# Performance work log

Measured on AMD Instinct MI355X. Metric: run time of the kernel, lower is better.

Reference implementation:

```python
import math
import jax
import jax.numpy as jnp
import numpy as np
from jax import lax
from jax.scipy.special import digamma

EPS_RHO = 1e-12
EPS_LOG = 1e-8
BANDWIDTH_FACTOR = 1.06
MIN_BANDWIDTH = 1e-4


def setup_inputs() -> dict:
    key = jax.random.key(0)
    activity = jax.random.uniform(key, (1024, 64), dtype=jnp.float32)  # values in [0,1]
    return {"activity": activity, "k": 5}


def _knn_joint_entropy(activity, k):
    B, N = activity.shape
    # (B, B, N) pairwise differences -> squared distances (B, B)
    diff = activity[:, None, :] - activity[None, :, :]
    dists_sq = jnp.sum(diff * diff, axis=-1)
    # k+1 smallest per row (includes self-distance 0); torch.topk(largest=False) ascending
    neg_topk, _ = lax.top_k(-dists_sq, k + 1)
    rho_sq = jnp.maximum(-neg_topk[:, k], EPS_RHO)
    # log unit-ball volume via lgamma (avoids overflow for large N)
    log_c_d = 0.5 * N * math.log(math.pi) - math.lgamma(N / 2 + 1)
    dg_k = digamma(jnp.float32(k))
    dg_B = digamma(jnp.float32(B))
    log_rho_sum = 0.5 * jnp.mean(jnp.log(rho_sq))
    h_nats = -dg_k + dg_B + log_c_d + N * log_rho_sum
    return h_nats / math.log(2.0)


def _kde_density(samples, query_points, bandwidth_factor):
    B_samples, R = samples.shape
    std = jnp.std(samples, axis=0, ddof=1)  # torch.std uses unbiased (ddof=1)
    h = jnp.maximum(bandwidth_factor * std * B_samples ** (-0.2), MIN_BANDWIDTH)  # (R,)
    X = query_points[:, None, :]  # (B, 1, R)
    Y = samples[None, :, :]       # (1, B, R)
    hr = h[None, None, :]
    norm_factor = math.sqrt(2 * math.pi)
    u_orig = (X - Y) / hr
    u_left = (X + Y) / hr
    u_right = (X - (2.0 - Y)) / hr
    kernel = (jnp.exp(-0.5 * u_orig ** 2)
              + jnp.exp(-0.5 * u_left ** 2)
              + jnp.exp(-0.5 * u_right ** 2)) / norm_factor
    density = jnp.sum(kernel, axis=1) / (B_samples * h[None, :])  # (B, R)
    return density


def _kde_marginal_entropies(activity, bandwidth_factor):
    density = _kde_density(activity, activity, bandwidth_factor)
    log_prob = jnp.log(density + EPS_LOG)
    return -jnp.mean(log_prob, axis=0)  # (R,)


def reference(activity, k):
    joint_h = _knn_joint_entropy(activity, k)            # scalar (bits)
    marginals = _kde_marginal_entropies(activity, BANDWIDTH_FACTOR)  # (N,)
    return jnp.concatenate([joint_h[None], marginals])   # (N+1,)
```

## Files before the change

### kernel.cpp

```cpp
#include <hip/hip_runtime.h>
#include <math.h>

#define BB 1024
#define NN 64

#define LN2F 0.69314718055994530942f
#define BINS 256
#define TW   64
#define HSIZE 769
#define NOUT 258
#define OBASE 255

__global__ __launch_bounds__(256, 4) void fused_kernel(const float* __restrict__ act,
                                                       const int* __restrict__ kptr,
                                                       float* __restrict__ logrho,
                                                       float* __restrict__ partial) {
    const int bx = blockIdx.x;
    const int tid = threadIdx.x;

    __shared__ float s_d[4096];
    __shared__ float s_x[264];

    if (bx < 256) {
        const int qbase = bx * 4;
        if (tid < 64) {
            ((float4*)s_x)[tid] = ((const float4*)(act + (size_t)qbase * NN))[tid];
        }
        __syncthreads();

        #pragma unroll 1
        for (int c = 0; c < 4; ++c) {
            const int j = tid + 256 * c;
            const float4* row = (const float4*)(act + (size_t)j * NN);
            float a0 = 0.f, a1 = 0.f, a2 = 0.f, a3 = 0.f;
            #pragma unroll 2
            for (int d = 0; d < 16; ++d) {
                const float4 v = row[d];
                {   const float4 qq = ((const float4*)s_x)[d];
                    float x0 = v.x - qq.x, x1 = v.y - qq.y, x2 = v.z - qq.z, x3 = v.w - qq.w;
                    a0 += x0 * x0 + x1 * x1 + x2 * x2 + x3 * x3; }
                {   const float4 qq = ((const float4*)s_x)[16 + d];
                    float x0 = v.x - qq.x, x1 = v.y - qq.y, x2 = v.z - qq.z, x3 = v.w - qq.w;
                    a1 += x0 * x0 + x1 * x1 + x2 * x2 + x3 * x3; }
                {   const float4 qq = ((const float4*)s_x)[32 + d];
                    float x0 = v.x - qq.x, x1 = v.y - qq.y, x2 = v.z - qq.z, x3 = v.w - qq.w;
                    a2 += x0 * x0 + x1 * x1 + x2 * x2 + x3 * x3; }
                {   const float4 qq = ((const float4*)s_x)[48 + d];
                    float x0 = v.x - qq.x, x1 = v.y - qq.y, x2 = v.z - qq.z, x3 = v.w - qq.w;
                    a3 += x0 * x0 + x1 * x1 + x2 * x2 + x3 * x3; }
            }
            s_d[0 * 1024 + j] = a0;
            s_d[1 * 1024 + j] = a1;
            s_d[2 * 1024 + j] = a2;
            s_d[3 * 1024 + j] = a3;
        }
        __syncthreads();

        const int w = tid >> 6, lane = tid & 63;
        float v[16];
        #pragma unroll
        for (int c = 0; c < 16; ++c) v[c] = s_d[w * 1024 + lane + 64 * c];
        const int kk = kptr[0];
        float last = 0.f;
        for (int e = 0; e <= kk; ++e) {
            float bv = 1e30f; int bi = 0;
            #pragma unroll
            for (int c = 0; c < 16; ++c) { if (v[c] < bv) { bv = v[c]; bi = c; } }
            float mv = bv; int mi = (lane << 4) | bi;
            #pragma unroll
            for (int off = 32; off > 0; off >>= 1) {
                float ov = __shfl_xor(mv, off);
                int   oi = __shfl_xor(mi, off);
                if (ov < mv || (ov == mv && oi < mi)) { mv = ov; mi = oi; }
            }
            last = mv;
            if ((mi >> 4) == lane) v[mi & 15] = 1e30f;
        }
        if (lane == 0) {
            logrho[qbase + w] = __builtin_amdgcn_logf(fmaxf(last, 1e-12f)) * LN2F;
        }
    } else {
        const int idx = bx - 256;
        const int r = idx >> 2;
        const int chunk = idx & 3;

        int*   hint = (int*)s_d;
        float* harr = s_d;
        float* ktab = s_d + 772;
        float* outg = s_d + 840;

        float cv[4];
        float lsum = 0.f, lsq = 0.f;
        #pragma unroll
        for (int c = 0; c < 4; ++c) {
            const int j = tid + 256 * c;
            float v = act[(size_t)j * NN + r];
            cv[c] = v;
            lsum += v; lsq += v * v;
        }
        #pragma unroll
        for (int off = 32; off > 0; off >>= 1) {
            lsum += __shfl_xor(lsum, off);
            lsq  += __shfl_xor(lsq,  off);
        }
        const int wid = tid >> 6;
        if ((tid & 63) == 0) { s_x[wid] = lsum; s_x[4 + wid] = lsq; }

        for (int i = tid; i < HSIZE; i += 256) hint[i] = 0;
        __syncthreads();

        const float total = s_x[0] + s_x[1] + s_x[2] + s_x[3];
        const float totsq = s_x[4] + s_x[5] + s_x[6] + s_x[7];
        const float mean = total * (1.f / BB);
        const float var = (totsq - (float)BB * mean * mean) * (1.f / (BB - 1));
        const float stdv = sqrtf(fmaxf(var, 0.f));
        const float h = fmaxf(1.06f * 0.25f * stdv, 1e-4f);
        const float ih = 1.f / h;
        const float a  = 0.84932180028801904272f * ih;
        const float ad = a * (1.f / (float)BINS);

        #pragma unroll
        for (int c = 0; c < 4; ++c) {
            const float x = cv[c];
            int b0 = (int)floorf(x * (float)BINS) + BINS;
            int b1 = (int)floorf(-x * (float)BINS) + BINS;
            int b2 = (int)floorf((2.f - x) * (float)BINS) + BINS;
            b0 = min(max(b0, 0), HSIZE - 1);
            b1 = min(max(b1, 0), HSIZE - 1);
            b2 = min(max(b2, 0), HSIZE - 1);
            atomicAdd(&hint[b0], 1);
            atomicAdd(&hint[b1], 1);
            atomicAdd(&hint[b2], 1);
        }
        if (tid <= TW) {
            const float t = ad * (float)tid;
            ktab[tid] = __builtin_amdgcn_exp2f(-(t * t));
        }
        __syncthreads();

        for (int i = tid; i < HSIZE; i += 256) {
            const int c = hint[i];
            harr[i] = (float)c;
        }
        __syncthreads();

        for (int o = tid; o < NOUT; o += 256) {
            const float* hp = harr + OBASE + o;
            float acc = hp[0] * ktab[0];
            #pragma unroll 4
            for (int m = 1; m <= TW; ++m)
                acc += (hp[m] + hp[-m]) * ktab[m];
            outg[o] = acc;
        }
        __syncthreads();

        const float dscale = 0.39894228040143267794f * ih * (1.f / (float)BB);
        const float x = cv[chunk];
        const float u = fmaf(x, (float)BINS, (float)OBASE + 0.5f);
        const float fu = floorf(u);
        const int i0 = (int)fu - OBASE;
        const float f = u - fu;
        const float dv = outg[i0] + (outg[i0 + 1] - outg[i0]) * f;
        float lp = __builtin_amdgcn_logf(fmaf(dv, dscale, 1e-8f)) * LN2F;

        #pragma unroll
        for (int off = 32; off > 0; off >>= 1) lp += __shfl_xor(lp, off);
        if ((tid & 63) == 0) s_x[8 + wid] = lp;
        __syncthreads();
        if (tid == 0) {
            partial[idx] = s_x[8] + s_x[9] + s_x[10] + s_x[11];
        }
    }
}

__global__ __launch_bounds__(256) void finalize_kernel(const float* __restrict__ logrho,
                                                       const float* __restrict__ partial,
                                                       const int* __restrict__ kptr,
                                                       double log_c_d, double dg_B,
                                                       float* __restrict__ out) {
    const int tid = threadIdx.x;
    __shared__ double red[256];

    double s = 0.0;
    #pragma unroll
    for (int c = 0; c < 4; ++c) s += (double)logrho[tid + 256 * c];
    red[tid] = s;
    __syncthreads();
    for (int st = 128; st > 0; st >>= 1) { if (tid < st) red[tid] += red[tid + st]; __syncthreads(); }

    if (tid == 0) {
        const int kk = kptr[0];
        double dgk = -0.57721566490153286061;
        for (int t = 1; t < kk; ++t) dgk += 1.0 / (double)t;
        const double log_rho_sum = 0.5 * (red[0] / (double)BB);
        const double h_nats = -dgk + dg_B + log_c_d + (double)NN * log_rho_sum;
        out[0] = (float)(h_nats / 0.69314718055994530942);
    }
    if (tid < NN) {
        const float p = partial[tid * 4 + 0] + partial[tid * 4 + 1]
                      + partial[tid * 4 + 2] + partial[tid * 4 + 3];
        out[1 + tid] = -p * (1.0f / (float)BB);
    }
}

extern "C" void kernel_launch(void* const* d_in, const int* in_sizes, int n_in,
                              void* d_out, int out_size, void* d_ws, size_t ws_size,
                              hipStream_t stream) {
    const float* act = (const float*)d_in[0];
    const int* kptr = (const int*)d_in[1];
    float* out = (float*)d_out;

    float* logrho = (float*)d_ws;
    float* partial = logrho + BB;

    const double log_c_d = 0.5 * (double)NN * log(M_PI) - lgamma((double)NN / 2.0 + 1.0);
    const double xB = (double)BB;
    const double dg_B = log(xB) - 1.0 / (2.0 * xB) - 1.0 / (12.0 * xB * xB)
                        + 1.0 / (120.0 * xB * xB * xB * xB);

    fused_kernel<<<512, 256, 0, stream>>>(act, kptr, logrho, partial);
    finalize_kernel<<<1, 256, 0, stream>>>(logrho, partial, kptr, log_c_d, dg_B, out);
}
```

Baseline: 22.58 us.

## Fold finalize into main kernel via last-block atomic counter; interleave row loads

Removes the separate finalize kernel launch. Each block increments a global counter, and the last block to finish does the final reduction, reading the per-block values through atomic loads. A memsetAsync is added to reset the counter. The distance loop is also restructured so each thread loads four rows in the same iteration with float4 accumulators, instead of four sequential passes, to expose more memory-level parallelism at the cost of more registers.

```diff
diff --git a/kernel.cpp b/kernel.cpp
--- a/kernel.cpp
+++ b/kernel.cpp
@@ -11,10 +11,15 @@
 #define NOUT 258
 #define OBASE 255
 
+#define NBLOCKS 512
+
 __global__ __launch_bounds__(256, 4) void fused_kernel(const float* __restrict__ act,
                                                        const int* __restrict__ kptr,
                                                        float* __restrict__ logrho,
-                                                       float* __restrict__ partial) {
+                                                       float* __restrict__ partial,
+                                                       int* __restrict__ counter,
+                                                       float* __restrict__ out,
+                                                       double log_c_d, double dg_B) {
     const int bx = blockIdx.x;
     const int tid = threadIdx.x;
 
@@ -28,32 +33,52 @@
         }
         __syncthreads();
 
-        #pragma unroll 1
-        for (int c = 0; c < 4; ++c) {
-            const int j = tid + 256 * c;
-            const float4* row = (const float4*)(act + (size_t)j * NN);
-            float a0 = 0.f, a1 = 0.f, a2 = 0.f, a3 = 0.f;
-            #pragma unroll 2
-            for (int d = 0; d < 16; ++d) {
-                const float4 v = row[d];
-                {   const float4 qq = ((const float4*)s_x)[d];
-                    float x0 = v.x - qq.x, x1 = v.y - qq.y, x2 = v.z - qq.z, x3 = v.w - qq.w;
-                    a0 += x0 * x0 + x1 * x1 + x2 * x2 + x3 * x3; }
-                {   const float4 qq = ((const float4*)s_x)[16 + d];
-                    float x0 = v.x - qq.x, x1 = v.y - qq.y, x2 = v.z - qq.z, x3 = v.w - qq.w;
-                    a1 += x0 * x0 + x1 * x1 + x2 * x2 + x3 * x3; }
-                {   const float4 qq = ((const float4*)s_x)[32 + d];
-                    float x0 = v.x - qq.x, x1 = v.y - qq.y, x2 = v.z - qq.z, x3 = v.w - qq.w;
-                    a2 += x0 * x0 + x1 * x1 + x2 * x2 + x3 * x3; }
-                {   const float4 qq = ((const float4*)s_x)[48 + d];
-                    float x0 = v.x - qq.x, x1 = v.y - qq.y, x2 = v.z - qq.z, x3 = v.w - qq.w;
-                    a3 += x0 * x0 + x1 * x1 + x2 * x2 + x3 * x3; }
-            }
-            s_d[0 * 1024 + j] = a0;
-            s_d[1 * 1024 + j] = a1;
-            s_d[2 * 1024 + j] = a2;
-            s_d[3 * 1024 + j] = a3;
-        }
+        const float4* qf = (const float4*)s_x;
+        float4 acc0 = {0,0,0,0}, acc1 = {0,0,0,0}, acc2 = {0,0,0,0}, acc3 = {0,0,0,0};
+        const float4* row0 = (const float4*)(act + (size_t)(tid + 0)   * NN);
+        const float4* row1 = (const float4*)(act + (size_t)(tid + 256) * NN);
+        const float4* row2 = (const float4*)(act + (size_t)(tid + 512) * NN);
+        const float4* row3 = (const float4*)(act + (size_t)(tid + 768) * NN);
+
+        #pragma unroll 2
+        for (int d = 0; d < 16; ++d) {
+            const float4 q0 = qf[d];
+            const float4 q1 = qf[16 + d];
+            const float4 q2 = qf[32 + d];
+            const float4 q3 = qf[48 + d];
+            {   const float4 v = row0[d];
+                float x,y,z,w;
+                x=v.x-q0.x; y=v.y-q0.y; z=v.z-q0.z; w=v.w-q0.w; acc0.x += x*x+y*y+z*z+w*w;
+                x=v.x-q1.x; y=v.y-q1.y; z=v.z-q1.z; w=v.w-q1.w; acc0.y += x*x+y*y+z*z+w*w;
+                x=v.x-q2.x; y=v.y-q2.y; z=v.z-q2.z; w=v.w-q2.w; acc0.z += x*x+y*y+z*z+w*w;
+                x=v.x-q3.x; y=v.y-q3.y; z=v.z-q3.z; w=v.w-q3.w; acc0.w += x*x+y*y+z*z+w*w; }
+            {   const float4 v = row1[d];
+                float x,y,z,w;
+                x=v.x-q0.x; y=v.y-q0.y; z=v.z-q0.z; w=v.w-q0.w; acc1.x += x*x+y*y+z*z+w*w;
+                x=v.x-q1.x; y=v.y-q1.y; z=v.z-q1.z; w=v.w-q1.w; acc1.y += x*x+y*y+z*z+w*w;
+                x=v.x-q2.x; y=v.y-q2.y; z=v.z-q2.z; w=v.w-q2.w; acc1.z += x*x+y*y+z*z+w*w;
+                x=v.x-q3.x; y=v.y-q3.y; z=v.z-q3.z; w=v.w-q3.w; acc1.w += x*x+y*y+z*z+w*w; }
+            {   const float4 v = row2[d];
+                float x,y,z,w;
+                x=v.x-q0.x; y=v.y-q0.y; z=v.z-q0.z; w=v.w-q0.w; acc2.x += x*x+y*y+z*z+w*w;
+                x=v.x-q1.x; y=v.y-q1.y; z=v.z-q1.z; w=v.w-q1.w; acc2.y += x*x+y*y+z*z+w*w;
+                x=v.x-q2.x; y=v.y-q2.y; z=v.z-q2.z; w=v.w-q2.w; acc2.z += x*x+y*y+z*z+w*w;
+                x=v.x-q3.x; y=v.y-q3.y; z=v.z-q3.z; w=v.w-q3.w; acc2.w += x*x+y*y+z*z+w*w; }
+            {   const float4 v = row3[d];
+                float x,y,z,w;
+                x=v.x-q0.x; y=v.y-q0.y; z=v.z-q0.z; w=v.w-q0.w; acc3.x += x*x+y*y+z*z+w*w;
+                x=v.x-q1.x; y=v.y-q1.y; z=v.z-q1.z; w=v.w-q1.w; acc3.y += x*x+y*y+z*z+w*w;
+                x=v.x-q2.x; y=v.y-q2.y; z=v.z-q2.z; w=v.w-q2.w; acc3.z += x*x+y*y+z*z+w*w;
+                x=v.x-q3.x; y=v.y-q3.y; z=v.z-q3.z; w=v.w-q3.w; acc3.w += x*x+y*y+z*z+w*w; }
+        }
+        s_d[0*1024 + tid +   0] = acc0.x;  s_d[1*1024 + tid +   0] = acc0.y;
+        s_d[2*1024 + tid +   0] = acc0.z;  s_d[3*1024 + tid +   0] = acc0.w;
+        s_d[0*1024 + tid + 256] = acc1.x;  s_d[1*1024 + tid + 256] = acc1.y;
+        s_d[2*1024 + tid + 256] = acc1.z;  s_d[3*1024 + tid + 256] = acc1.w;
+        s_d[0*1024 + tid + 512] = acc2.x;  s_d[1*1024 + tid + 512] = acc2.y;
+        s_d[2*1024 + tid + 512] = acc2.z;  s_d[3*1024 + tid + 512] = acc2.w;
+        s_d[0*1024 + tid + 768] = acc3.x;  s_d[1*1024 + tid + 768] = acc3.y;
+        s_d[2*1024 + tid + 768] = acc3.z;  s_d[3*1024 + tid + 768] = acc3.w;
         __syncthreads();
 
         const int w = tid >> 6, lane = tid & 63;
@@ -171,34 +196,37 @@
             partial[idx] = s_x[8] + s_x[9] + s_x[10] + s_x[11];
         }
     }
-}
-
-__global__ __launch_bounds__(256) void finalize_kernel(const float* __restrict__ logrho,
-                                                       const float* __restrict__ partial,
-                                                       const int* __restrict__ kptr,
-                                                       double log_c_d, double dg_B,
-                                                       float* __restrict__ out) {
-    const int tid = threadIdx.x;
-    __shared__ double red[256];
+
+    __syncthreads();
+    __threadfence();
+    if (tid == 0) ((int*)s_x)[0] = atomicAdd(counter, 1);
+    __syncthreads();
+    if (((int*)s_x)[0] != NBLOCKS - 1) return;
+
+    __threadfence();
+    double* dred = (double*)s_d;
 
     double s = 0.0;
     #pragma unroll
-    for (int c = 0; c < 4; ++c) s += (double)logrho[tid + 256 * c];
-    red[tid] = s;
+    for (int c = 0; c < 4; ++c)
+        s += (double)atomicAdd(&logrho[tid + 256 * c], 0.0f);
+    dred[tid] = s;
     __syncthreads();
-    for (int st = 128; st > 0; st >>= 1) { if (tid < st) red[tid] += red[tid + st]; __syncthreads(); }
+    for (int st = 128; st > 0; st >>= 1) { if (tid < st) dred[tid] += dred[tid + st]; __syncthreads(); }
 
     if (tid == 0) {
         const int kk = kptr[0];
         double dgk = -0.57721566490153286061;
         for (int t = 1; t < kk; ++t) dgk += 1.0 / (double)t;
-        const double log_rho_sum = 0.5 * (red[0] / (double)BB);
+        const double log_rho_sum = 0.5 * (dred[0] / (double)BB);
         const double h_nats = -dgk + dg_B + log_c_d + (double)NN * log_rho_sum;
         out[0] = (float)(h_nats / 0.69314718055994530942);
     }
     if (tid < NN) {
-        const float p = partial[tid * 4 + 0] + partial[tid * 4 + 1]
-                      + partial[tid * 4 + 2] + partial[tid * 4 + 3];
+        float p = 0.f;
+        #pragma unroll
+        for (int c = 0; c < 4; ++c)
+            p += atomicAdd(&partial[tid * 4 + c], 0.0f);
         out[1 + tid] = -p * (1.0f / (float)BB);
     }
 }
@@ -210,14 +238,16 @@
     const int* kptr = (const int*)d_in[1];
     float* out = (float*)d_out;
 
-    float* logrho = (float*)d_ws;
+    float* logrho  = (float*)d_ws;
     float* partial = logrho + BB;
+    int*   counter = (int*)(partial + 256);
 
     const double log_c_d = 0.5 * (double)NN * log(M_PI) - lgamma((double)NN / 2.0 + 1.0);
     const double xB = (double)BB;
     const double dg_B = log(xB) - 1.0 / (2.0 * xB) - 1.0 / (12.0 * xB * xB)
                         + 1.0 / (120.0 * xB * xB * xB * xB);
 
-    fused_kernel<<<512, 256, 0, stream>>>(act, kptr, logrho, partial);
-    finalize_kernel<<<1, 256, 0, stream>>>(logrho, partial, kptr, log_c_d, dg_B, out);
+    hipMemsetAsync(counter, 0, sizeof(int), stream);
+    fused_kernel<<<NBLOCKS, 256, 0, stream>>>(act, kptr, logrho, partial, counter,
+                                              out, log_c_d, dg_B);
 }
```

Result: slower. 60.92 us (+169.8%).

## Fold finalize into main kernel via last-block atomic counter

Applied to the files above, without the earlier changes.

Removes the separate finalize kernel launch. Each block publishes its results with device-scope atomics and bumps a global counter, and the last block to finish does the final reductions. This saves one kernel launch and its gap, at the cost of a hipMemsetAsync to reset the counter, which is itself another stream operation, plus atomic traffic. Whether the launch overhead actually drops depends on whether the memset is cheaper than the kernel it replaces.

```diff
diff --git a/kernel.cpp b/kernel.cpp
--- a/kernel.cpp
+++ b/kernel.cpp
@@ -11,15 +11,21 @@
 #define NOUT 258
 #define OBASE 255
 
+#define NBLOCKS 512
+
 __global__ __launch_bounds__(256, 4) void fused_kernel(const float* __restrict__ act,
                                                        const int* __restrict__ kptr,
                                                        float* __restrict__ logrho,
-                                                       float* __restrict__ partial) {
+                                                       float* __restrict__ partial,
+                                                       unsigned int* __restrict__ counter,
+                                                       float* __restrict__ out,
+                                                       double log_c_d, double dg_B) {
     const int bx = blockIdx.x;
     const int tid = threadIdx.x;
 
     __shared__ float s_d[4096];
     __shared__ float s_x[264];
+    __shared__ int s_last;
 
     if (bx < 256) {
         const int qbase = bx * 4;
@@ -77,7 +83,9 @@
             if ((mi >> 4) == lane) v[mi & 15] = 1e30f;
         }
         if (lane == 0) {
-            logrho[qbase + w] = __builtin_amdgcn_logf(fmaxf(last, 1e-12f)) * LN2F;
+            const float lr = __builtin_amdgcn_logf(fmaxf(last, 1e-12f)) * LN2F;
+            float old = atomicExch(&logrho[qbase + w], lr);
+            asm volatile("" :: "v"(old));
         }
     } else {
         const int idx = bx - 256;
@@ -168,37 +176,44 @@
         if ((tid & 63) == 0) s_x[8 + wid] = lp;
         __syncthreads();
         if (tid == 0) {
-            partial[idx] = s_x[8] + s_x[9] + s_x[10] + s_x[11];
-        }
-    }
-}
-
-__global__ __launch_bounds__(256) void finalize_kernel(const float* __restrict__ logrho,
-                                                       const float* __restrict__ partial,
-                                                       const int* __restrict__ kptr,
-                                                       double log_c_d, double dg_B,
-                                                       float* __restrict__ out) {
-    const int tid = threadIdx.x;
-    __shared__ double red[256];
+            const float p = s_x[8] + s_x[9] + s_x[10] + s_x[11];
+            float old = atomicExch(&partial[idx], p);
+            asm volatile("" :: "v"(old));
+        }
+    }
+
+    __syncthreads();
+    if (tid == 0) {
+        asm volatile("s_waitcnt vmcnt(0)" ::: "memory");
+        const unsigned int old = atomicAdd(counter, 1u);
+        s_last = (old == NBLOCKS - 1u);
+    }
+    __syncthreads();
+    if (!s_last) return;
+
+    double* dred = (double*)s_d;
 
     double s = 0.0;
     #pragma unroll
-    for (int c = 0; c < 4; ++c) s += (double)logrho[tid + 256 * c];
-    red[tid] = s;
+    for (int c = 0; c < 4; ++c)
+        s += (double)atomicAdd(&logrho[tid + 256 * c], 0.0f);
+    dred[tid] = s;
     __syncthreads();
-    for (int st = 128; st > 0; st >>= 1) { if (tid < st) red[tid] += red[tid + st]; __syncthreads(); }
+    for (int st = 128; st > 0; st >>= 1) { if (tid < st) dred[tid] += dred[tid + st]; __syncthreads(); }
 
     if (tid == 0) {
         const int kk = kptr[0];
         double dgk = -0.57721566490153286061;
         for (int t = 1; t < kk; ++t) dgk += 1.0 / (double)t;
-        const double log_rho_sum = 0.5 * (red[0] / (double)BB);
+        const double log_rho_sum = 0.5 * (dred[0] / (double)BB);
         const double h_nats = -dgk + dg_B + log_c_d + (double)NN * log_rho_sum;
         out[0] = (float)(h_nats / 0.69314718055994530942);
     }
     if (tid < NN) {
-        const float p = partial[tid * 4 + 0] + partial[tid * 4 + 1]
-                      + partial[tid * 4 + 2] + partial[tid * 4 + 3];
+        float p = 0.f;
+        #pragma unroll
+        for (int c = 0; c < 4; ++c)
+            p += atomicAdd(&partial[tid * 4 + c], 0.0f);
         out[1 + tid] = -p * (1.0f / (float)BB);
     }
 }
@@ -210,14 +225,16 @@
     const int* kptr = (const int*)d_in[1];
     float* out = (float*)d_out;
 
-    float* logrho = (float*)d_ws;
+    float* logrho  = (float*)d_ws;
     float* partial = logrho + BB;
+    unsigned int* counter = (unsigned int*)(partial + 256);
 
     const double log_c_d = 0.5 * (double)NN * log(M_PI) - lgamma((double)NN / 2.0 + 1.0);
     const double xB = (double)BB;
     const double dg_B = log(xB) - 1.0 / (2.0 * xB) - 1.0 / (12.0 * xB * xB)
                         + 1.0 / (120.0 * xB * xB * xB * xB);
 
-    fused_kernel<<<512, 256, 0, stream>>>(act, kptr, logrho, partial);
-    finalize_kernel<<<1, 256, 0, stream>>>(logrho, partial, kptr, log_c_d, dg_B, out);
+    hipMemsetAsync(counter, 0, sizeof(unsigned int), stream);
+    fused_kernel<<<NBLOCKS, 256, 0, stream>>>(act, kptr, logrho, partial, counter,
+                                              out, log_c_d, dg_B);
 }
```

Result: slower. 30.06 us (+33.1%).
